# Kernel tuning notes

Measured on AMD Instinct MI355X. Metric: run time of the kernel, lower is better.

## Reference

```python
import jax, jax.numpy as jnp
import numpy as np

EMBED_DIM = 1024
NUM_HEADS = 16
HEAD_DIM = EMBED_DIM // NUM_HEADS


def setup_inputs() -> dict:
    key = jax.random.key(0)
    kx, kw1, kb1, kw2, kb2 = jax.random.split(key, 5)
    B, T, C = 4, 2048, EMBED_DIM
    s = 1.0 / np.sqrt(C)
    return {
        "x": jax.random.normal(kx, (B, T, C), dtype=jnp.float32),
        "qkv_w": jax.random.normal(kw1, (3 * C, C), dtype=jnp.float32) * s,
        "qkv_b": jax.random.normal(kb1, (3 * C,), dtype=jnp.float32) * 0.01,
        "proj_w": jax.random.normal(kw2, (C, C), dtype=jnp.float32) * s,
        "proj_b": jax.random.normal(kb2, (C,), dtype=jnp.float32) * 0.01,
    }


def reference(x, qkv_w, qkv_b, proj_w, proj_b):
    B, T, C = x.shape
    H, D = NUM_HEADS, HEAD_DIM
    qkv = jnp.einsum('btc,oc->bto', x, qkv_w) + qkv_b  # [B,T,3C]
    q, k, v = jnp.split(qkv, 3, axis=-1)
    def heads(t):
        return t.reshape(B, T, H, D).transpose(0, 2, 1, 3)  # [B,H,T,D]
    q, k, v = heads(q), heads(k), heads(v)
    scale = 1.0 / jnp.sqrt(jnp.asarray(D, dtype=x.dtype))
    att = jnp.einsum('bhqd,bhkd->bhqk', q, k) * scale  # [B,H,T,T]
    causal = jnp.tril(jnp.ones((T, T), dtype=bool))
    att = jnp.where(causal, att, -jnp.inf)
    att = jax.nn.softmax(att, axis=-1)
    out = jnp.einsum('bhqk,bhkd->bhqd', att, v)  # [B,H,T,D]
    out = out.transpose(0, 2, 1, 3).reshape(B, T, C)
    out = jnp.einsum('btc,oc->bto', out, proj_w) + proj_b
    return out
```

## Files before the change

### kernel.cpp

```cpp
#include <hip/hip_runtime.h>
#include <hip/hip_bf16.h>

typedef __bf16 bf16x8 __attribute__((ext_vector_type(8)));
typedef __bf16 bf16x4 __attribute__((ext_vector_type(4)));
typedef float  f32x4  __attribute__((ext_vector_type(4)));

#define MFMA16(a, b, c) __builtin_amdgcn_mfma_f32_16x16x32_bf16((a), (b), (c), 0, 0, 0)
#define GLD16(g, l)                                                              \
    __builtin_amdgcn_global_load_lds(                                            \
        (const __attribute__((address_space(1))) void*)(g),                      \
        (__attribute__((address_space(3))) void*)(l), 16, 0, 0)

__global__ __launch_bounds__(256) void cvt3_f32_bf16(const float* __restrict__ a, __bf16* __restrict__ oa, int na,
                                                     const float* __restrict__ b, __bf16* __restrict__ ob, int nb,
                                                     const float* __restrict__ c, __bf16* __restrict__ oc, int nc) {
    const int stride = gridDim.x * blockDim.x * 4;
    const int start = (blockIdx.x * blockDim.x + threadIdx.x) * 4;
    for (int i = start; i < na; i += stride) {
        float4 v = *(const float4*)(a + i);
        bf16x4 o; o[0] = (__bf16)v.x; o[1] = (__bf16)v.y; o[2] = (__bf16)v.z; o[3] = (__bf16)v.w;
        *(bf16x4*)(oa + i) = o;
    }
    for (int i = start; i < nb; i += stride) {
        float4 v = *(const float4*)(b + i);
        bf16x4 o; o[0] = (__bf16)v.x; o[1] = (__bf16)v.y; o[2] = (__bf16)v.z; o[3] = (__bf16)v.w;
        *(bf16x4*)(ob + i) = o;
    }
    for (int i = start; i < nc; i += stride) {
        float4 v = *(const float4*)(c + i);
        bf16x4 o; o[0] = (__bf16)v.x; o[1] = (__bf16)v.y; o[2] = (__bf16)v.z; o[3] = (__bf16)v.w;
        *(bf16x4*)(oc + i) = o;
    }
}

__global__ __launch_bounds__(256, 2) void qkv_gemm(const __bf16* __restrict__ X,
                                                   const __bf16* __restrict__ W,
                                                   const float* __restrict__ bias,
                                                   __bf16* __restrict__ Qo,
                                                   __bf16* __restrict__ Kf,
                                                   __bf16* __restrict__ Vf) {
    const int KD = 1024;
    __shared__ __align__(16) char smem[34816];
    __bf16* As = (__bf16*)smem;
    __bf16* Bs = (__bf16*)(smem + 8192);
    const int tid = threadIdx.x;
    const int lane = tid & 63, w = tid >> 6;
    const int lr = lane & 15, lg = lane >> 4;
    const int orig = blockIdx.x;
    const int wgid = (orig & 7) * 192 + (orig >> 3);
    const int row0 = (wgid & 63) * 128, col0 = (wgid >> 6) * 128;
    const int wrow = (w >> 1) * 64, wcol = (w & 1) * 64;
    f32x4 acc[4][4] = {};
    const int c0 = tid, c1 = tid + 256;
    const __bf16* ga0 = X + (size_t)(row0 + (c0 >> 2)) * KD + (c0 & 3) * 8;
    const __bf16* ga1 = X + (size_t)(row0 + (c1 >> 2)) * KD + (c1 & 3) * 8;
    const __bf16* gb0 = W + (size_t)(col0 + (c0 >> 2)) * KD + (c0 & 3) * 8;
    const __bf16* gb1 = W + (size_t)(col0 + (c1 >> 2)) * KD + (c1 & 3) * 8;
    for (int k0 = 0; k0 < KD; k0 += 32) {
        __syncthreads();
        GLD16(ga0 + k0, As + c0 * 8);
        GLD16(ga1 + k0, As + c1 * 8);
        GLD16(gb0 + k0, Bs + c0 * 8);
        GLD16(gb1 + k0, Bs + c1 * 8);
        __syncthreads();
        bf16x8 a[4], b[4];
#pragma unroll
        for (int mi = 0; mi < 4; mi++)
            a[mi] = *(const bf16x8*)&As[(wrow + mi * 16 + lr) * 32 + lg * 8];
#pragma unroll
        for (int ni = 0; ni < 4; ni++)
            b[ni] = *(const bf16x8*)&Bs[(wcol + ni * 16 + lr) * 32 + lg * 8];
#pragma unroll
        for (int mi = 0; mi < 4; mi++)
#pragma unroll
            for (int ni = 0; ni < 4; ni++)
                acc[mi][ni] = MFMA16(a[mi], b[ni], acc[mi][ni]);
    }

    if (col0 < 1024) {
#pragma unroll
        for (int mi = 0; mi < 4; mi++)
#pragma unroll
            for (int ni = 0; ni < 4; ni++)
#pragma unroll
                for (int r = 0; r < 4; r++) {
                    int m = row0 + wrow + mi * 16 + lg * 4 + r;
                    int n = col0 + wcol + ni * 16 + lr;
                    float v = acc[mi][ni][r] + bias[n];
                    int b_ = m >> 11, t = m & 2047;
                    int c = n & 1023;
                    int bh = b_ * 16 + (c >> 6), d = c & 63;
                    Qo[(size_t)(bh * 2048 + t) * 64 + d] = (__bf16)(v * 0.125f);
                }
    } else if (col0 < 2048) {
#pragma unroll
        for (int mi = 0; mi < 4; mi++)
#pragma unroll
            for (int ni = 0; ni < 4; ni++)
#pragma unroll
                for (int r = 0; r < 4; r++) {
                    int m = row0 + wrow + mi * 16 + lg * 4 + r;
                    int n = col0 + wcol + ni * 16 + lr;
                    float v = acc[mi][ni][r] + bias[n];
                    int b_ = m >> 11, t = m & 2047;
                    int c = n & 1023;
                    int bh = b_ * 16 + (c >> 6), d = c & 63;
                    size_t flat = (((size_t)bh * 128 + (t >> 4)) * 2 + (d >> 5)) * 512
                                + (((d & 31) >> 3) * 16 + (t & 15)) * 8 + (d & 7);
                    Kf[flat] = (__bf16)v;
                }
    } else {
        __syncthreads();
        __bf16* vt = (__bf16*)smem;
#pragma unroll
        for (int mi = 0; mi < 4; mi++)
#pragma unroll
            for (int ni = 0; ni < 4; ni++) {
                int cl = wcol + ni * 16 + lr;
                int tl = wrow + mi * 16 + lg * 4;
                int n = col0 + cl;
                bf16x4 pk;
#pragma unroll
                for (int r = 0; r < 4; r++)
                    pk[r] = (__bf16)(acc[mi][ni][r] + bias[n]);
                *(bf16x4*)&vt[cl * 136 + tl] = pk;
            }
        __syncthreads();
        const int b_ = row0 >> 11, t_base = row0 & 2047;
        const int lane2 = tid & 63, w2 = tid >> 6;
        const int lr2 = lane2 & 15, lg2 = lane2 >> 4;
#pragma unroll
        for (int g = 0; g < 8; g++) {
            int group = g * 4 + w2;
            int hh2 = group >> 4;
            int k32l = (group >> 2) & 3;
            int dt = group & 3;
            const __bf16* src = &vt[(hh2 * 64 + dt * 16 + lr2) * 136 + k32l * 32 + lg2 * 8];
            int c = (col0 & 1023) + hh2 * 64;
            int bh = b_ * 16 + (c >> 6);
            int kt32 = (t_base >> 5) + k32l;
            __bf16* dst = Vf + ((((size_t)bh * 64 + kt32) * 4 + dt) * 512) + lane2 * 8;
            *(bf16x8*)dst = *(const bf16x8*)src;
        }
    }
}

__global__ __launch_bounds__(256) void attn_kernel(const __bf16* __restrict__ Q,
                                                   const __bf16* __restrict__ Kf,
                                                   const __bf16* __restrict__ Vf,
                                                   __bf16* __restrict__ ATT) {
    const int T = 2048, D = 64;
    __shared__ __align__(16) __bf16 plds[4][32][68];
    const int lane = threadIdx.x & 63, w = threadIdx.x >> 6;
    const int lr = lane & 15, lg = lane >> 4;
    const int orig = blockIdx.x;
    const int wgid = (orig & 7) * 64 + (orig >> 3);
    const int bh = wgid >> 3;
    const int idx = (wgid & 7) * 4 + w;
    const int b_ = bh >> 4, hh = bh & 15;
    const __bf16* Qp  = Q  + (size_t)bh * T * D;
    const __bf16* Kfp = Kf + (size_t)bh * 131072;
    const __bf16* Vfp = Vf + (size_t)bh * 131072;

    for (int ph = 0; ph < 2; ++ph) {
        const int j = ph ? 63 - idx : idx;
        const int qrow0 = j * 32;
        bf16x8 qa[2][2];
#pragma unroll
        for (int qt = 0; qt < 2; qt++)
#pragma unroll
            for (int dk = 0; dk < 2; dk++)
                qa[qt][dk] = *(const bf16x8*)(Qp + (size_t)(qrow0 + qt * 16 + lr) * D + dk * 32 + lg * 8);

        float mrow[2][4], lsum[2][4];
#pragma unroll
        for (int qt = 0; qt < 2; qt++)
#pragma unroll
            for (int r = 0; r < 4; r++) { mrow[qt][r] = -1e30f; lsum[qt][r] = 0.f; }
        f32x4 o[2][4] = {};

        const int nkb = (j + 2) >> 1;

        auto tileBody = [&](int kt0, bool masked) {
            const int kb = kt0 * 64;
            bf16x8 kf[4][2];
#pragma unroll
            for (int kt = 0; kt < 4; kt++)
#pragma unroll
                for (int dk = 0; dk < 2; dk++)
                    kf[kt][dk] = *(const bf16x8*)(Kfp + (((kt0 * 4 + kt) * 2 + dk) << 9) + lane * 8);
            f32x4 s[2][4] = {};
#pragma unroll
            for (int qt = 0; qt < 2; qt++)
#pragma unroll
                for (int kt = 0; kt < 4; kt++)
#pragma unroll
                    for (int dk = 0; dk < 2; dk++)
                        s[qt][kt] = MFMA16(qa[qt][dk], kf[kt][dk], s[qt][kt]);

            float lmax[2][4];
            int flag = 0;
#pragma unroll
            for (int qt = 0; qt < 2; qt++)
#pragma unroll
                for (int r = 0; r < 4; r++) {
                    const int qq = qrow0 + qt * 16 + lg * 4 + r;
                    float mt = -1e30f;
#pragma unroll
                    for (int kt = 0; kt < 4; kt++) {
                        float v = s[qt][kt][r];
                        if (masked) v = (kb + kt * 16 + lr <= qq) ? v : -1e30f;
                        s[qt][kt][r] = v;
                        mt = fmaxf(mt, v);
                    }
                    lmax[qt][r] = mt;
                    flag |= (mt > mrow[qt][r] + 8.0f) ? 1 : 0;
                }

            if (__any(flag)) {
#pragma unroll
                for (int qt = 0; qt < 2; qt++)
#pragma unroll
                    for (int r = 0; r < 4; r++) {
                        float mt = lmax[qt][r];
#pragma unroll
                        for (int off = 1; off < 16; off <<= 1)
                            mt = fmaxf(mt, __shfl_xor(mt, off));
                        float mnew = fmaxf(mrow[qt][r], mt);
                        float al = __expf(mrow[qt][r] - mnew);
                        mrow[qt][r] = mnew;
                        lsum[qt][r] *= al;
#pragma unroll
                        for (int dt = 0; dt < 4; dt++) o[qt][dt][r] *= al;
                    }
            }

#pragma unroll
            for (int qt = 0; qt < 2; qt++)
#pragma unroll
                for (int r = 0; r < 4; r++) {
                    float rs = 0.f;
#pragma unroll
                    for (int kt = 0; kt < 4; kt++) {
                        float p = __expf(s[qt][kt][r] - mrow[qt][r]);
                        s[qt][kt][r] = p;
                        rs += p;
                    }
                    lsum[qt][r] += rs;
                }

#pragma unroll
            for (int qt = 0; qt < 2; qt++)
#pragma unroll
                for (int kt = 0; kt < 4; kt++)
#pragma unroll
                    for (int r = 0; r < 4; r++)
                        plds[w][qt * 16 + lg * 4 + r][kt * 16 + lr] = (__bf16)s[qt][kt][r];

            bf16x8 pa[2][2];
#pragma unroll
            for (int qt = 0; qt < 2; qt++)
#pragma unroll
                for (int kh = 0; kh < 2; kh++)
                    pa[qt][kh] = *(const bf16x8*)&plds[w][qt * 16 + lr][kh * 32 + lg * 8];

#pragma unroll
            for (int kh = 0; kh < 2; kh++) {
                bf16x8 vf[4];
#pragma unroll
                for (int dt = 0; dt < 4; dt++)
                    vf[dt] = *(const bf16x8*)(Vfp + ((((kt0 * 2 + kh) * 4) + dt) << 9) + lane * 8);
#pragma unroll
                for (int qt = 0; qt < 2; qt++)
#pragma unroll
                    for (int dt = 0; dt < 4; dt++)
                        o[qt][dt] = MFMA16(pa[qt][kh], vf[dt], o[qt][dt]);
            }
        };

        for (int kt0 = 0; kt0 < nkb - 1; ++kt0)
            tileBody(kt0, false);
        tileBody(nkb - 1, true);

#pragma unroll
        for (int qt = 0; qt < 2; qt++)
#pragma unroll
            for (int r = 0; r < 4; r++) {
                float rs = lsum[qt][r];
#pragma unroll
                for (int off = 1; off < 16; off <<= 1)
                    rs += __shfl_xor(rs, off);
                lsum[qt][r] = 1.0f / rs;
            }
#pragma unroll
        for (int qt = 0; qt < 2; qt++)
#pragma unroll
            for (int dt = 0; dt < 4; dt++)
#pragma unroll
                for (int r = 0; r < 4; r++) {
                    int qq = qrow0 + qt * 16 + lg * 4 + r;
                    int dd = dt * 16 + lr;
                    float val = o[qt][dt][r] * lsum[qt][r];
                    ATT[(size_t)(b_ * 2048 + qq) * 1024 + hh * 64 + dd] = (__bf16)val;
                }
    }
}

__global__ __launch_bounds__(256, 2) void proj_gemm(const __bf16* __restrict__ A,
                                                    const __bf16* __restrict__ W,
                                                    const float* __restrict__ bias,
                                                    float* __restrict__ out) {
    const int KD = 1024;
    __shared__ __align__(16) __bf16 As[128 * 32];
    __shared__ __align__(16) __bf16 Bs[128 * 32];
    const int tid = threadIdx.x;
    const int lane = tid & 63, w = tid >> 6;
    const int lr = lane & 15, lg = lane >> 4;
    const int orig = blockIdx.x;
    const int wgid = (orig & 7) * 64 + (orig >> 3);
    const int row0 = (wgid & 63) * 128, col0 = (wgid >> 6) * 128;
    const int wrow = (w >> 1) * 64, wcol = (w & 1) * 64;
    f32x4 acc[4][4] = {};
    const int c0 = tid, c1 = tid + 256;
    const __bf16* ga0 = A + (size_t)(row0 + (c0 >> 2)) * KD + (c0 & 3) * 8;
    const __bf16* ga1 = A + (size_t)(row0 + (c1 >> 2)) * KD + (c1 & 3) * 8;
    const __bf16* gb0 = W + (size_t)(col0 + (c0 >> 2)) * KD + (c0 & 3) * 8;
    const __bf16* gb1 = W + (size_t)(col0 + (c1 >> 2)) * KD + (c1 & 3) * 8;
    for (int k0 = 0; k0 < KD; k0 += 32) {
        __syncthreads();
        GLD16(ga0 + k0, As + c0 * 8);
        GLD16(ga1 + k0, As + c1 * 8);
        GLD16(gb0 + k0, Bs + c0 * 8);
        GLD16(gb1 + k0, Bs + c1 * 8);
        __syncthreads();
        bf16x8 a[4], b[4];
#pragma unroll
        for (int mi = 0; mi < 4; mi++)
            a[mi] = *(const bf16x8*)&As[(wrow + mi * 16 + lr) * 32 + lg * 8];
#pragma unroll
        for (int ni = 0; ni < 4; ni++)
            b[ni] = *(const bf16x8*)&Bs[(wcol + ni * 16 + lr) * 32 + lg * 8];
#pragma unroll
        for (int mi = 0; mi < 4; mi++)
#pragma unroll
            for (int ni = 0; ni < 4; ni++)
                acc[mi][ni] = MFMA16(a[mi], b[ni], acc[mi][ni]);
    }
#pragma unroll
    for (int mi = 0; mi < 4; mi++)
#pragma unroll
        for (int ni = 0; ni < 4; ni++)
#pragma unroll
            for (int r = 0; r < 4; r++) {
                int m = row0 + wrow + mi * 16 + lg * 4 + r;
                int n = col0 + wcol + ni * 16 + lr;
                out[(size_t)m * 1024 + n] = acc[mi][ni][r] + bias[n];
            }
}

extern "C" void kernel_launch(void* const* d_in, const int* in_sizes, int n_in,
                              void* d_out, int out_size, void* d_ws, size_t ws_size,
                              hipStream_t stream) {
    const float* x      = (const float*)d_in[0];
    const float* qkv_w  = (const float*)d_in[1];
    const float* qkv_b  = (const float*)d_in[2];
    const float* proj_w = (const float*)d_in[3];
    const float* proj_b = (const float*)d_in[4];
    float* out = (float*)d_out;
    char* ws = (char*)d_ws;

    __bf16* xb    = (__bf16*)(ws);
    __bf16* wqkv  = (__bf16*)(ws + 16777216);
    __bf16* wproj = (__bf16*)(ws + 23068672);
    __bf16* qb    = (__bf16*)(ws + 25165824);
    __bf16* kfb   = (__bf16*)(ws + 41943040);
    __bf16* vfb   = (__bf16*)(ws + 58720256);
    __bf16* attb  = xb;

    cvt3_f32_bf16<<<2048, 256, 0, stream>>>(x, xb, 4 * 2048 * 1024,
                                            qkv_w, wqkv, 3072 * 1024,
                                            proj_w, wproj, 1024 * 1024);
    qkv_gemm<<<1536, 256, 0, stream>>>(xb, wqkv, qkv_b, qb, kfb, vfb);
    attn_kernel<<<512, 256, 0, stream>>>(qb, kfb, vfb, attb);
    proj_gemm<<<512, 256, 0, stream>>>(attb, wproj, proj_b, out);
}
```

Baseline: 191.3 us.

## Widen attention key tile to 128 and use exp2 with log2e-folded Q scale

The attention inner loop now processes 128 keys per tile instead of 64. This halves the number of online-softmax max and rescale steps per query block and gives more independent MFMAs between reductions. The Q scaling constant now folds log2(e) into 1/sqrt(D), so exp2f can replace __expf in the softmax. In exchange, register pressure roughly doubles for the score tile and the LDS footprint for P doubles. The causal last tile also wastes more masked work, since the number of key blocks is now (j>>2)+1 for 32-row query blocks.

```diff
diff --git a/kernel.cpp b/kernel.cpp
--- a/kernel.cpp
+++ b/kernel.cpp
@@ -90,7 +90,7 @@
                     int b_ = m >> 11, t = m & 2047;
                     int c = n & 1023;
                     int bh = b_ * 16 + (c >> 6), d = c & 63;
-                    Qo[(size_t)(bh * 2048 + t) * 64 + d] = (__bf16)(v * 0.125f);
+                    Qo[(size_t)(bh * 2048 + t) * 64 + d] = (__bf16)(v * 0.18033688f);
                 }
     } else if (col0 < 2048) {
 #pragma unroll
@@ -150,7 +150,7 @@
                                                    const __bf16* __restrict__ Vf,
                                                    __bf16* __restrict__ ATT) {
     const int T = 2048, D = 64;
-    __shared__ __align__(16) __bf16 plds[4][32][68];
+    __shared__ __align__(16) __bf16 plds[4][2][32][68];
     const int lane = threadIdx.x & 63, w = threadIdx.x >> 6;
     const int lr = lane & 15, lg = lane >> 4;
     const int orig = blockIdx.x;
@@ -179,24 +179,41 @@
             for (int r = 0; r < 4; r++) { mrow[qt][r] = -1e30f; lsum[qt][r] = 0.f; }
         f32x4 o[2][4] = {};
 
-        const int nkb = (j + 2) >> 1;
+        const int nkb = (j >> 2) + 1;
 
         auto tileBody = [&](int kt0, bool masked) {
-            const int kb = kt0 * 64;
-            bf16x8 kf[4][2];
-#pragma unroll
-            for (int kt = 0; kt < 4; kt++)
-#pragma unroll
-                for (int dk = 0; dk < 2; dk++)
-                    kf[kt][dk] = *(const bf16x8*)(Kfp + (((kt0 * 4 + kt) * 2 + dk) << 9) + lane * 8);
-            f32x4 s[2][4] = {};
-#pragma unroll
-            for (int qt = 0; qt < 2; qt++)
+            const int kb = kt0 * 128;
+            f32x4 s[2][8] = {};
+            {
+                bf16x8 kf[4][2];
 #pragma unroll
                 for (int kt = 0; kt < 4; kt++)
 #pragma unroll
                     for (int dk = 0; dk < 2; dk++)
-                        s[qt][kt] = MFMA16(qa[qt][dk], kf[kt][dk], s[qt][kt]);
+                        kf[kt][dk] = *(const bf16x8*)(Kfp + (((kt0 * 8 + kt) * 2 + dk) << 9) + lane * 8);
+#pragma unroll
+                for (int qt = 0; qt < 2; qt++)
+#pragma unroll
+                    for (int kt = 0; kt < 4; kt++)
+#pragma unroll
+                        for (int dk = 0; dk < 2; dk++)
+                            s[qt][kt] = MFMA16(qa[qt][dk], kf[kt][dk], s[qt][kt]);
+            }
+            {
+                bf16x8 kf[4][2];
+#pragma unroll
+                for (int kt = 0; kt < 4; kt++)
+#pragma unroll
+                    for (int dk = 0; dk < 2; dk++)
+                        kf[kt][dk] = *(const bf16x8*)(Kfp + (((kt0 * 8 + 4 + kt) * 2 + dk) << 9) + lane * 8);
+#pragma unroll
+                for (int qt = 0; qt < 2; qt++)
+#pragma unroll
+                    for (int kt = 0; kt < 4; kt++)
+#pragma unroll
+                        for (int dk = 0; dk < 2; dk++)
+                            s[qt][4 + kt] = MFMA16(qa[qt][dk], kf[kt][dk], s[qt][4 + kt]);
+            }
 
             float lmax[2][4];
             int flag = 0;
@@ -207,7 +224,7 @@
                     const int qq = qrow0 + qt * 16 + lg * 4 + r;
                     float mt = -1e30f;
 #pragma unroll
-                    for (int kt = 0; kt < 4; kt++) {
+                    for (int kt = 0; kt < 8; kt++) {
                         float v = s[qt][kt][r];
                         if (masked) v = (kb + kt * 16 + lr <= qq) ? v : -1e30f;
                         s[qt][kt][r] = v;
@@ -227,7 +244,7 @@
                         for (int off = 1; off < 16; off <<= 1)
                             mt = fmaxf(mt, __shfl_xor(mt, off));
                         float mnew = fmaxf(mrow[qt][r], mt);
-                        float al = __expf(mrow[qt][r] - mnew);
+                        float al = exp2f(mrow[qt][r] - mnew);
                         mrow[qt][r] = mnew;
                         lsum[qt][r] *= al;
 #pragma unroll
@@ -241,8 +258,8 @@
                 for (int r = 0; r < 4; r++) {
                     float rs = 0.f;
 #pragma unroll
-                    for (int kt = 0; kt < 4; kt++) {
-                        float p = __expf(s[qt][kt][r] - mrow[qt][r]);
+                    for (int kt = 0; kt < 8; kt++) {
+                        float p = exp2f(s[qt][kt][r] - mrow[qt][r]);
                         s[qt][kt][r] = p;
                         rs += p;
                     }
@@ -252,29 +269,26 @@
 #pragma unroll
             for (int qt = 0; qt < 2; qt++)
 #pragma unroll
-                for (int kt = 0; kt < 4; kt++)
+                for (int kt = 0; kt < 8; kt++)
 #pragma unroll
                     for (int r = 0; r < 4; r++)
-                        plds[w][qt * 16 + lg * 4 + r][kt * 16 + lr] = (__bf16)s[qt][kt][r];
-
-            bf16x8 pa[2][2];
-#pragma unroll
-            for (int qt = 0; qt < 2; qt++)
-#pragma unroll
-                for (int kh = 0; kh < 2; kh++)
-                    pa[qt][kh] = *(const bf16x8*)&plds[w][qt * 16 + lr][kh * 32 + lg * 8];
-
-#pragma unroll
-            for (int kh = 0; kh < 2; kh++) {
+                        plds[w][kt >> 2][qt * 16 + lg * 4 + r][(kt & 3) * 16 + lr] = (__bf16)s[qt][kt][r];
+
+#pragma unroll
+            for (int ks = 0; ks < 4; ks++) {
                 bf16x8 vf[4];
 #pragma unroll
                 for (int dt = 0; dt < 4; dt++)
-                    vf[dt] = *(const bf16x8*)(Vfp + ((((kt0 * 2 + kh) * 4) + dt) << 9) + lane * 8);
+                    vf[dt] = *(const bf16x8*)(Vfp + ((((kt0 * 4 + ks) * 4) + dt) << 9) + lane * 8);
+                bf16x8 pa[2];
 #pragma unroll
                 for (int qt = 0; qt < 2; qt++)
+                    pa[qt] = *(const bf16x8*)&plds[w][ks >> 1][qt * 16 + lr][(ks & 1) * 32 + lg * 8];
+#pragma unroll
+                for (int qt = 0; qt < 2; qt++)
 #pragma unroll
                     for (int dt = 0; dt < 4; dt++)
-                        o[qt][dt] = MFMA16(pa[qt][kh], vf[dt], o[qt][dt]);
+                        o[qt][dt] = MFMA16(pa[qt], vf[dt], o[qt][dt]);
             }
         };
 
```

Measured after the change: 238.5 us. +24.7%, slower.

## Double GEMM K-tile to 64 with XOR-swizzled LDS and switch softmax to exp2

Applied to the files above, without the earlier changes.

Both the QKV and projection GEMMs now load a 64-wide K slice per iteration instead of 32. This halves the number of barrier pairs, and the LDS layout uses an XOR swizzle on 16-byte chunks to avoid bank conflicts on the wider rows. The Q scale now folds in log2(e), so the attention softmax can use exp2f instead of __expf. The changes trade more LDS per block and more live registers for fewer synchronizations, with a risk of lower occupancy.

```diff
diff --git a/kernel.cpp b/kernel.cpp
--- a/kernel.cpp
+++ b/kernel.cpp
@@ -42,7 +42,7 @@
     const int KD = 1024;
     __shared__ __align__(16) char smem[34816];
     __bf16* As = (__bf16*)smem;
-    __bf16* Bs = (__bf16*)(smem + 8192);
+    __bf16* Bs = (__bf16*)(smem + 16384);
     const int tid = threadIdx.x;
     const int lane = tid & 63, w = tid >> 6;
     const int lr = lane & 15, lg = lane >> 4;
@@ -51,30 +51,40 @@
     const int row0 = (wgid & 63) * 128, col0 = (wgid >> 6) * 128;
     const int wrow = (w >> 1) * 64, wcol = (w & 1) * 64;
     f32x4 acc[4][4] = {};
-    const int c0 = tid, c1 = tid + 256;
-    const __bf16* ga0 = X + (size_t)(row0 + (c0 >> 2)) * KD + (c0 & 3) * 8;
-    const __bf16* ga1 = X + (size_t)(row0 + (c1 >> 2)) * KD + (c1 & 3) * 8;
-    const __bf16* gb0 = W + (size_t)(col0 + (c0 >> 2)) * KD + (c0 & 3) * 8;
-    const __bf16* gb1 = W + (size_t)(col0 + (c1 >> 2)) * KD + (c1 & 3) * 8;
-    for (int k0 = 0; k0 < KD; k0 += 32) {
-        __syncthreads();
-        GLD16(ga0 + k0, As + c0 * 8);
-        GLD16(ga1 + k0, As + c1 * 8);
-        GLD16(gb0 + k0, Bs + c0 * 8);
-        GLD16(gb1 + k0, Bs + c1 * 8);
-        __syncthreads();
-        bf16x8 a[4], b[4];
-#pragma unroll
-        for (int mi = 0; mi < 4; mi++)
-            a[mi] = *(const bf16x8*)&As[(wrow + mi * 16 + lr) * 32 + lg * 8];
-#pragma unroll
-        for (int ni = 0; ni < 4; ni++)
-            b[ni] = *(const bf16x8*)&Bs[(wcol + ni * 16 + lr) * 32 + lg * 8];
-#pragma unroll
-        for (int mi = 0; mi < 4; mi++)
+    const __bf16* gaG[4];
+    const __bf16* gbG[4];
+#pragma unroll
+    for (int i = 0; i < 4; i++) {
+        int c = tid + i * 256, r = c >> 3, u = (c & 7) ^ (r & 7);
+        gaG[i] = X + (size_t)(row0 + r) * KD + u * 8;
+        gbG[i] = W + (size_t)(col0 + r) * KD + u * 8;
+    }
+    const int uX = lr & 7;
+    for (int k0 = 0; k0 < KD; k0 += 64) {
+        __syncthreads();
+#pragma unroll
+        for (int i = 0; i < 4; i++) GLD16(gaG[i] + k0, As + (tid + i * 256) * 8);
+#pragma unroll
+        for (int i = 0; i < 4; i++) GLD16(gbG[i] + k0, Bs + (tid + i * 256) * 8);
+        __syncthreads();
+        bf16x8 a[4][2], b[4][2];
+#pragma unroll
+        for (int ks = 0; ks < 2; ks++) {
+            const int u = (ks * 4 + lg) ^ uX;
+#pragma unroll
+            for (int mi = 0; mi < 4; mi++)
+                a[mi][ks] = *(const bf16x8*)&As[(wrow + mi * 16 + lr) * 64 + u * 8];
 #pragma unroll
             for (int ni = 0; ni < 4; ni++)
-                acc[mi][ni] = MFMA16(a[mi], b[ni], acc[mi][ni]);
+                b[ni][ks] = *(const bf16x8*)&Bs[(wcol + ni * 16 + lr) * 64 + u * 8];
+        }
+#pragma unroll
+        for (int ks = 0; ks < 2; ks++)
+#pragma unroll
+            for (int mi = 0; mi < 4; mi++)
+#pragma unroll
+                for (int ni = 0; ni < 4; ni++)
+                    acc[mi][ni] = MFMA16(a[mi][ks], b[ni][ks], acc[mi][ni]);
     }
 
     if (col0 < 1024) {
@@ -90,7 +100,7 @@
                     int b_ = m >> 11, t = m & 2047;
                     int c = n & 1023;
                     int bh = b_ * 16 + (c >> 6), d = c & 63;
-                    Qo[(size_t)(bh * 2048 + t) * 64 + d] = (__bf16)(v * 0.125f);
+                    Qo[(size_t)(bh * 2048 + t) * 64 + d] = (__bf16)(v * 0.18033688f);
                 }
     } else if (col0 < 2048) {
 #pragma unroll
@@ -227,7 +237,7 @@
                         for (int off = 1; off < 16; off <<= 1)
                             mt = fmaxf(mt, __shfl_xor(mt, off));
                         float mnew = fmaxf(mrow[qt][r], mt);
-                        float al = __expf(mrow[qt][r] - mnew);
+                        float al = exp2f(mrow[qt][r] - mnew);
                         mrow[qt][r] = mnew;
                         lsum[qt][r] *= al;
 #pragma unroll
@@ -242,7 +252,7 @@
                     float rs = 0.f;
 #pragma unroll
                     for (int kt = 0; kt < 4; kt++) {
-                        float p = __expf(s[qt][kt][r] - mrow[qt][r]);
+                        float p = exp2f(s[qt][kt][r] - mrow[qt][r]);
                         s[qt][kt][r] = p;
                         rs += p;
                     }
@@ -311,8 +321,8 @@
                                                     const float* __restrict__ bias,
                                                     float* __restrict__ out) {
     const int KD = 1024;
-    __shared__ __align__(16) __bf16 As[128 * 32];
-    __shared__ __align__(16) __bf16 Bs[128 * 32];
+    __shared__ __align__(16) __bf16 As[128 * 64];
+    __shared__ __align__(16) __bf16 Bs[128 * 64];
     const int tid = threadIdx.x;
     const int lane = tid & 63, w = tid >> 6;
     const int lr = lane & 15, lg = lane >> 4;
@@ -321,30 +331,40 @@
     const int row0 = (wgid & 63) * 128, col0 = (wgid >> 6) * 128;
     const int wrow = (w >> 1) * 64, wcol = (w & 1) * 64;
     f32x4 acc[4][4] = {};
-    const int c0 = tid, c1 = tid + 256;
-    const __bf16* ga0 = A + (size_t)(row0 + (c0 >> 2)) * KD + (c0 & 3) * 8;
-    const __bf16* ga1 = A + (size_t)(row0 + (c1 >> 2)) * KD + (c1 & 3) * 8;
-    const __bf16* gb0 = W + (size_t)(col0 + (c0 >> 2)) * KD + (c0 & 3) * 8;
-    const __bf16* gb1 = W + (size_t)(col0 + (c1 >> 2)) * KD + (c1 & 3) * 8;
-    for (int k0 = 0; k0 < KD; k0 += 32) {
-        __syncthreads();
-        GLD16(ga0 + k0, As + c0 * 8);
-        GLD16(ga1 + k0, As + c1 * 8);
-        GLD16(gb0 + k0, Bs + c0 * 8);
-        GLD16(gb1 + k0, Bs + c1 * 8);
-        __syncthreads();
-        bf16x8 a[4], b[4];
-#pragma unroll
-        for (int mi = 0; mi < 4; mi++)
-            a[mi] = *(const bf16x8*)&As[(wrow + mi * 16 + lr) * 32 + lg * 8];
-#pragma unroll
-        for (int ni = 0; ni < 4; ni++)
-            b[ni] = *(const bf16x8*)&Bs[(wcol + ni * 16 + lr) * 32 + lg * 8];
-#pragma unroll
-        for (int mi = 0; mi < 4; mi++)
+    const __bf16* gaG[4];
+    const __bf16* gbG[4];
+#pragma unroll
+    for (int i = 0; i < 4; i++) {
+        int c = tid + i * 256, r = c >> 3, u = (c & 7) ^ (r & 7);
+        gaG[i] = A + (size_t)(row0 + r) * KD + u * 8;
+        gbG[i] = W + (size_t)(col0 + r) * KD + u * 8;
+    }
+    const int uX = lr & 7;
+    for (int k0 = 0; k0 < KD; k0 += 64) {
+        __syncthreads();
+#pragma unroll
+        for (int i = 0; i < 4; i++) GLD16(gaG[i] + k0, As + (tid + i * 256) * 8);
+#pragma unroll
+        for (int i = 0; i < 4; i++) GLD16(gbG[i] + k0, Bs + (tid + i * 256) * 8);
+        __syncthreads();
+        bf16x8 a[4][2], b[4][2];
+#pragma unroll
+        for (int ks = 0; ks < 2; ks++) {
+            const int u = (ks * 4 + lg) ^ uX;
+#pragma unroll
+            for (int mi = 0; mi < 4; mi++)
+                a[mi][ks] = *(const bf16x8*)&As[(wrow + mi * 16 + lr) * 64 + u * 8];
 #pragma unroll
             for (int ni = 0; ni < 4; ni++)
-                acc[mi][ni] = MFMA16(a[mi], b[ni], acc[mi][ni]);
+                b[ni][ks] = *(const bf16x8*)&Bs[(wcol + ni * 16 + lr) * 64 + u * 8];
+        }
+#pragma unroll
+        for (int ks = 0; ks < 2; ks++)
+#pragma unroll
+            for (int mi = 0; mi < 4; mi++)
+#pragma unroll
+                for (int ni = 0; ni < 4; ni++)
+                    acc[mi][ni] = MFMA16(a[mi][ks], b[ni][ks], acc[mi][ni]);
     }
 #pragma unroll
     for (int mi = 0; mi < 4; mi++)
```

New measurement: 199.5 us. +4.3%, slower.
